# Kernel optimization log

Hardware: AMD Instinct MI355X
Metric: run time of the kernel (lower is better)

## Reference

```python
import math
import jax, jax.numpy as jnp
import numpy as np

N, E, D, H, NH, DH, EIN, EOUT, G = 30000, 480000, 128, 128, 4, 32, 16, 16, 64
EPS = 1e-5

def _leaky(x):
    return jax.nn.leaky_relu(x, 0.01)

def _graph_norm(x, batch, w, b, a):
    # torch_geometric GraphNorm: out = w * (x - a*mean) / sqrt(var + eps) + b, stats per graph
    cnt = jnp.maximum(jax.ops.segment_sum(jnp.ones((x.shape[0],), x.dtype), batch, num_segments=G), 1.0)[:, None]
    mean = jax.ops.segment_sum(x, batch, num_segments=G) / cnt
    out = x - a * mean[batch]
    var = jax.ops.segment_sum(out * out, batch, num_segments=G) / cnt
    return w * out / jnp.sqrt(var + EPS)[batch] + b

def setup_inputs() -> dict:
    key = jax.random.key(0)
    ks = jax.random.split(key, 24)
    lin = lambda k, di, do: jax.random.normal(k, (di, do), jnp.float32) * 0.02
    z = lambda d: jnp.zeros((d,), jnp.float32)
    o = lambda d: jnp.ones((d,), jnp.float32)
    return {
        "node": jax.random.normal(ks[0], (N, D), jnp.float32),
        "edge": jax.random.normal(ks[1], (E, EIN), jnp.float32),
        "coords": jax.random.normal(ks[2], (N, 3), jnp.float32),
        "Ws": lin(ks[3], D, H), "bs": z(H),
        "Wd": lin(ks[4], D, H), "bd": z(H),
        "Wv": lin(ks[5], D, H), "bv": z(H),
        "We1": lin(ks[6], EIN + 1, H), "be1": z(H),
        "We2": lin(ks[7], H, H), "be2": z(H),
        "Wun": lin(ks[8], H, H), "bun": z(H),
        "Wue": lin(ks[9], H, EOUT), "bue": z(EOUT),
        "Wg": lin(ks[10], 3 * H, H), "bg": z(H),
        "Wf1": lin(ks[11], H, H), "bf1": z(H),
        "Wf2": lin(ks[12], H, H), "bf2": z(H),
        "gn1_w": o(H), "gn1_b": z(H), "gn1_a": o(H),
        "gn2_w": o(H), "gn2_b": z(H), "gn2_a": o(H),
        "edge_index": jax.random.randint(ks[13], (2, E), 0, N),
        "batch": jnp.sort(jax.random.randint(ks[14], (N,), 0, G)),
    }

def reference(node, edge, coords, Ws, bs, Wd, bd, Wv, bv, We1, be1, We2, be2,
              Wun, bun, Wue, bue, Wg, bg, Wf1, bf1, Wf2, bf2,
              gn1_w, gn1_b, gn1_a, gn2_w, gn2_b, gn2_a, edge_index, batch):
    i, j = edge_index[0], edge_index[1]
    src = node @ Ws + bs              # [N,H]
    dst = node @ Wd + bd
    value = node @ Wv + bv
    d = coords[i] - coords[j]
    dist = jnp.sqrt(jnp.sum(d * d, axis=-1, keepdims=True) + 1e-12) * 0.1
    e = jnp.concatenate([edge, dist], axis=-1)            # [E, EIN+1]
    e = _leaky(e @ We1 + be1) @ We2 + be2                   # edge_layer (dropout=identity in eval)
    edge_key = src[j] * e
    edge_result = (dst[i] * edge_key / math.sqrt(DH)).reshape(E, NH, DH)
    scores = jnp.sum(jnp.abs(edge_result), axis=2)         # L1 norm over dh -> [E,NH]
    smax = jax.ops.segment_max(scores, i, num_segments=N)  # scatter softmax over dst nodes
    ex = jnp.exp(scores - smax[i])
    den = jax.ops.segment_sum(ex, i, num_segments=N)
    ew = (ex / den[i])[..., None]                           # [E,NH,1]
    agg = jax.ops.segment_sum(ew * value[j].reshape(E, NH, DH), i, num_segments=N).reshape(N, H)
    node_new = agg @ Wun + bun
    edge_new = edge_result.reshape(E, H) @ Wue + bue
    g = jax.nn.sigmoid(jnp.concatenate([node_new, node, node_new - node], axis=-1) @ Wg + bg)
    n1 = _graph_norm(g * node_new + node, batch, gn1_w, gn1_b, gn1_a)
    fx = _leaky(n1 @ Wf1 + bf1) @ Wf2 + bf2                 # fix_node
    n2 = _graph_norm(g * fx + n1, batch, gn2_w, gn2_b, gn2_a)
    return (n2, edge_new, coords)
```

## Files before the change

kernel.cpp:

```cpp
#include <hip/hip_runtime.h>
#include <hip/hip_bf16.h>

#define NN_ 30000
#define NE_ 480000
#define DIM 128
#define EINF 16
#define EOUTF 16
#define NG 64
#define RSQRT_DH 0.17677669529663687f

typedef unsigned short u16;
typedef __attribute__((ext_vector_type(8))) short short8;
typedef __attribute__((ext_vector_type(8))) unsigned short ushort8v;
typedef __attribute__((ext_vector_type(4))) float floatx4;

#define W_DEG     0
#define W_CUR     30000
#define W_GSUM1   60000
#define W_GSQ1    68192
#define W_GSUM2   76384
#define W_GSQ2    84576
#define W_ZEND    92768
#define W_OFF     92768
#define W_BSUM    122772
#define W_GSTART  122900
#define W_EID     122968
#define W_JC      602968
#define W_SCORES  1082968
#define W_SRCB    3002968
#define W_DSTB    4922968
#define W_VALB    6842968
#define W_A       8762968
#define W_B       12602968
#define W_C       16442968
#define W_WGC     20282968
#define W_WE2B    20315736
#define W_WPROJ   20323928

static __device__ __forceinline__ u16 f2bf(float x) {
  __hip_bfloat16 h = __float2bfloat16(x);
  return *reinterpret_cast<u16*>(&h);
}
static __device__ __forceinline__ float bf2f(u16 v) {
  unsigned int b = ((unsigned int)v) << 16;
  return __uint_as_float(b);
}

static __device__ __forceinline__ void stage32(const float* __restrict__ X,
                                               float* xsb, int row0, int tid) {
#pragma unroll
  for (int t = 0; t < 4; ++t) {
    int idx = tid + t * 256;
    int r = idx >> 5, c4 = (idx & 31) * 4;
    int row = row0 + r;
    float4 v; v.x = v.y = v.z = v.w = 0.f;
    if (row < NN_) v = *(const float4*)&X[(size_t)row * DIM + c4];
    *(float4*)&xsb[r * DIM + c4] = v;
  }
}

static __device__ __forceinline__ void mm_k128(const float* xsb, int ld,
                                               const float* __restrict__ W,
                                               float acc[4][4], int tid) {
  int cg = tid & 31, rg = tid >> 5;
  int c0 = cg * 4, r0 = rg * 4;
  for (int k = 0; k < 128; k += 4) {
    float4 w0 = *(const float4*)&W[(size_t)(k + 0) * DIM + c0];
    float4 w1 = *(const float4*)&W[(size_t)(k + 1) * DIM + c0];
    float4 w2 = *(const float4*)&W[(size_t)(k + 2) * DIM + c0];
    float4 w3 = *(const float4*)&W[(size_t)(k + 3) * DIM + c0];
#pragma unroll
    for (int u = 0; u < 4; ++u) {
      float4 xv = *(const float4*)&xsb[(r0 + u) * ld + k];
      acc[u][0] += xv.x * w0.x + xv.y * w1.x + xv.z * w2.x + xv.w * w3.x;
      acc[u][1] += xv.x * w0.y + xv.y * w1.y + xv.z * w2.y + xv.w * w3.y;
      acc[u][2] += xv.x * w0.z + xv.y * w1.z + xv.z * w2.z + xv.w * w3.z;
      acc[u][3] += xv.x * w0.w + xv.y * w1.w + xv.z * w2.w + xv.w * w3.w;
    }
  }
}

static __device__ __forceinline__ void tile_gn_stats(const float* xsb,
    const int* bg_s, int row0, int tid,
    float* __restrict__ gsum, float* __restrict__ gsq) {
  int c = tid & 127, half = tid >> 7;
  float sm = 0.f, sq = 0.f;
  int gcur = -1;
  for (int r = 0; r < 16; ++r) {
    int rl = half * 16 + r;
    int row = row0 + rl;
    if (row >= NN_) break;
    int g = bg_s[rl];
    float v = xsb[rl * DIM + c];
    if (g != gcur) {
      if (gcur >= 0) {
        atomicAdd(&gsum[gcur * DIM + c], sm);
        atomicAdd(&gsq[gcur * DIM + c], sq);
      }
      gcur = g; sm = 0.f; sq = 0.f;
    }
    sm += v; sq += v * v;
  }
  if (gcur >= 0) {
    atomicAdd(&gsum[gcur * DIM + c], sm);
    atomicAdd(&gsq[gcur * DIM + c], sq);
  }
}

__global__ void setup_kernel(const int* __restrict__ batch, int* __restrict__ gstart,
                             const float* __restrict__ Wg, float* __restrict__ Wgc,
                             const float* __restrict__ We2, u16* __restrict__ we2b,
                             const float* __restrict__ Ws, const float* __restrict__ Wd,
                             const float* __restrict__ Wv, u16* __restrict__ wproj) {
  int b = blockIdx.x, tid = threadIdx.x;
  if (b == 0) {
    int g = tid;
    if (g <= NG) {
      int lo = 0, hi = NN_;
      while (lo < hi) { int mid = (lo + hi) >> 1; if (batch[mid] < g) lo = mid + 1; else hi = mid; }
      gstart[g] = lo;
    }
  } else if (b < 129) {
    int idx = (b - 1) * 256 + tid;
    int k = idx >> 7, c = idx & 127;
    float v;
    if (k < 128) v = Wg[(size_t)k * DIM + c] + Wg[(size_t)(256 + k) * DIM + c];
    else { int kk = k - 128; v = Wg[(size_t)(128 + kk) * DIM + c] - Wg[(size_t)(256 + kk) * DIM + c]; }
    Wgc[idx] = v;
  } else if (b < 193) {
    int idx = (b - 129) * 256 + tid;
    int j = idx & 7, lane = (idx >> 3) & 63, s = (idx >> 9) & 3, T = idx >> 11;
    int k = s * 32 + ((lane >> 4) << 3) + j;
    int n = T * 16 + (lane & 15);
    we2b[idx] = f2bf(We2[(size_t)k * DIM + n]);
  } else {
    int idx = (b - 193) * 256 + tid;
    int which = idx >> 14;
    int sub = idx & 16383;
    int j = sub & 7, lane = (sub >> 3) & 63, s = (sub >> 9) & 3, T = sub >> 11;
    int k = s * 32 + ((lane >> 4) << 3) + j;
    int n = T * 16 + (lane & 15);
    int mat = which >> 1;
    const float* Wsrc = (mat == 0) ? Ws : (mat == 1) ? Wd : Wv;
    float w = Wsrc[(size_t)k * DIM + n];
    u16 h = f2bf(w);
    u16 o = (which & 1) ? f2bf(w - bf2f(h)) : h;
    wproj[which * 16384 + sub] = o;
  }
}

__global__ void deg_kernel(const int* __restrict__ EI, int* __restrict__ deg) {
  int e = blockIdx.x * 256 + threadIdx.x;
  if (e < NE_) atomicAdd(&deg[EI[e]], 1);
}

__global__ void __launch_bounds__(256) proj_kernel(
    const float* __restrict__ node, const u16* __restrict__ wproj,
    const float* __restrict__ bs, const float* __restrict__ bd,
    const float* __restrict__ bv,
    u16* __restrict__ srcb, u16* __restrict__ dstb, u16* __restrict__ valb) {
  __shared__ __align__(16) u16 ah[32 * 136];
  __shared__ __align__(16) u16 al[32 * 136];
  __shared__ __align__(16) float park[32 * 132];
  int tid = threadIdx.x, row0 = blockIdx.x * 32;
  int r2 = tid >> 3, c16 = (tid & 7) * 16;

  {
    int row = row0 + r2;
    float v[16];
    if (row < NN_) {
#pragma unroll
      for (int q = 0; q < 4; ++q) {
        float4 x = *(const float4*)&node[(size_t)row * DIM + c16 + q * 4];
        v[q * 4 + 0] = x.x; v[q * 4 + 1] = x.y;
        v[q * 4 + 2] = x.z; v[q * 4 + 3] = x.w;
      }
    } else {
#pragma unroll
      for (int q = 0; q < 16; ++q) v[q] = 0.f;
    }
#pragma unroll
    for (int h2 = 0; h2 < 2; ++h2) {
      ushort8v hh, ll;
#pragma unroll
      for (int q = 0; q < 8; ++q) {
        float x = v[h2 * 8 + q];
        u16 h = f2bf(x);
        hh[q] = h;
        ll[q] = f2bf(x - bf2f(h));
      }
      *(ushort8v*)&ah[r2 * 136 + c16 + h2 * 8] = hh;
      *(ushort8v*)&al[r2 * 136 + c16 + h2 * 8] = ll;
    }
  }
  __syncthreads();

  int wv_ = tid >> 6, lane = tid & 63;
  int mtile = wv_ & 1, nhalf = wv_ >> 1;
  int quad = lane >> 4, lrow = lane & 15;
  int m0 = mtile * 16;

  short8 afh[4], afl[4];
#pragma unroll
  for (int s = 0; s < 4; ++s) {
    afh[s] = *(const short8*)&ah[(m0 + lrow) * 136 + s * 32 + quad * 8];
    afl[s] = *(const short8*)&al[(m0 + lrow) * 136 + s * 32 + quad * 8];
  }

  const float* Bt[3] = {bs, bd, bv};
  u16* Yt[3] = {srcb, dstb, valb};
#pragma unroll 1
  for (int g3 = 0; g3 < 3; ++g3) {
    const u16* wh = wproj + (size_t)(g3 * 2 + 0) * 16384;
    const u16* wl = wproj + (size_t)(g3 * 2 + 1) * 16384;
    floatx4 dacc[4];
#pragma unroll
    for (int t = 0; t < 4; ++t) dacc[t] = (floatx4){0.f, 0.f, 0.f, 0.f};
#pragma unroll
    for (int s = 0; s < 4; ++s) {
#pragma unroll
      for (int t = 0; t < 4; ++t) {
        int T = nhalf * 4 + t;
        size_t off = (size_t)((T * 4 + s) * 64 + lane) * 8;
        short8 bh = *(const short8*)&wh[off];
        short8 bl = *(const short8*)&wl[off];
        dacc[t] = __builtin_amdgcn_mfma_f32_16x16x32_bf16(afh[s], bh, dacc[t], 0, 0, 0);
        dacc[t] = __builtin_amdgcn_mfma_f32_16x16x32_bf16(afl[s], bh, dacc[t], 0, 0, 0);
        dacc[t] = __builtin_amdgcn_mfma_f32_16x16x32_bf16(afh[s], bl, dacc[t], 0, 0, 0);
      }
    }
#pragma unroll
    for (int t = 0; t < 4; ++t) {
      int col = nhalf * 64 + t * 16 + lrow;
#pragma unroll
      for (int r = 0; r < 4; ++r)
        park[(m0 + quad * 4 + r) * 132 + col] = dacc[t][r];
    }
    __syncthreads();
    {
      int row = row0 + r2;
      if (row < NN_) {
#pragma unroll
        for (int h2 = 0; h2 < 2; ++h2) {
          ushort8v o;
#pragma unroll
          for (int q = 0; q < 8; ++q) {
            float pv = park[r2 * 132 + c16 + h2 * 8 + q] + Bt[g3][c16 + h2 * 8 + q];
            o[q] = f2bf(pv);
          }
          *(ushort8v*)&Yt[g3][(size_t)row * DIM + c16 + h2 * 8] = o;
        }
      }
    }
    __syncthreads();
  }
}

__global__ void __launch_bounds__(256) nnew_gate_kernel(
    const float* __restrict__ AGG, const float* __restrict__ NODE,
    const int* __restrict__ batch,
    const float* __restrict__ Wun, const float* __restrict__ bun,
    const float* __restrict__ Wgc, const float* __restrict__ bg,
    float* __restrict__ gsum1, float* __restrict__ gsq1,
    float* __restrict__ G, float* __restrict__ X1) {
  __shared__ __align__(16) float xs0[32 * DIM];
  __shared__ __align__(16) float xs1[32 * DIM];
  __shared__ int bg_s[32];
  int tid = threadIdx.x, row0 = blockIdx.x * 32;
  stage32(AGG, xs0, row0, tid);
  stage32(NODE, xs1, row0, tid);
  if (tid < 32) {
    int row = row0 + tid;
    bg_s[tid] = (row < NN_) ? batch[row] : 0;
  }
  __syncthreads();
  int cg = tid & 31, rg = tid >> 5, c0 = cg * 4, r0 = rg * 4;
  {
    float acc[4][4] = {};
    mm_k128(xs0, DIM, Wun, acc, tid);
    __syncthreads();
    float4 bv = *(const float4*)&bun[c0];
#pragma unroll
    for (int u = 0; u < 4; ++u) {
      float4 ov; ov.x = acc[u][0] + bv.x; ov.y = acc[u][1] + bv.y;
      ov.z = acc[u][2] + bv.z; ov.w = acc[u][3] + bv.w;
      *(float4*)&xs0[(r0 + u) * DIM + c0] = ov;
    }
  }
  __syncthreads();
  float acc[4][4] = {};
  mm_k128(xs0, DIM, Wgc, acc, tid);
  mm_k128(xs1, DIM, Wgc + 128 * DIM, acc, tid);
  float4 bv = *(const float4*)&bg[c0];
  float4 xvv[4];
#pragma unroll
  for (int u = 0; u < 4; ++u) {
    int row = row0 + r0 + u;
    float z0 = acc[u][0] + bv.x, z1 = acc[u][1] + bv.y;
    float z2 = acc[u][2] + bv.z, z3 = acc[u][3] + bv.w;
    float g0 = 1.f / (1.f + __expf(-z0));
    float g1 = 1.f / (1.f + __expf(-z1));
    float g2 = 1.f / (1.f + __expf(-z2));
    float g3 = 1.f / (1.f + __expf(-z3));
    float4 nn4 = *(const float4*)&xs0[(r0 + u) * DIM + c0];
    float4 nd4 = *(const float4*)&xs1[(r0 + u) * DIM + c0];
    float4 gv; gv.x = g0; gv.y = g1; gv.z = g2; gv.w = g3;
    float4 xv; xv.x = g0 * nn4.x + nd4.x; xv.y = g1 * nn4.y + nd4.y;
    xv.z = g2 * nn4.z + nd4.z; xv.w = g3 * nn4.w + nd4.w;
    xvv[u] = xv;
    if (row < NN_) {
      *(float4*)&G[(size_t)row * DIM + c0] = gv;
      *(float4*)&X1[(size_t)row * DIM + c0] = xv;
    }
  }
  __syncthreads();
#pragma unroll
  for (int u = 0; u < 4; ++u)
    *(float4*)&xs1[(r0 + u) * DIM + c0] = xvv[u];
  __syncthreads();
  tile_gn_stats(xs1, bg_s, row0, tid, gsum1, gsq1);
}

__global__ void __launch_bounds__(256) fx_kernel(
    const float* __restrict__ X1, const int* __restrict__ batch,
    const int* __restrict__ gstart,
    const float* __restrict__ gsum1, const float* __restrict__ gsq1,
    const float* __restrict__ g1w, const float* __restrict__ g1b,
    const float* __restrict__ g1a,
    const float* __restrict__ Wf1, const float* __restrict__ bf1,
    const float* __restrict__ Wf2, const float* __restrict__ bf2,
    const float* __restrict__ G,
    float* __restrict__ gsum2, float* __restrict__ gsq2,
    float* __restrict__ X2) {
  __shared__ __align__(16) float xs0[32 * DIM];
  __shared__ __align__(16) float xs1[32 * DIM];
  __shared__ int bg_s[32];
  int tid = threadIdx.x, row0 = blockIdx.x * 32;
  stage32(X1, xs0, row0, tid);
  if (tid < 32) {
    int row = row0 + tid;
    bg_s[tid] = (row < NN_) ? batch[row] : 0;
  }
  __syncthreads();
  int cg = tid & 31, rg = tid >> 5, c0 = cg * 4, r0 = rg * 4;
#pragma unroll
  for (int u = 0; u < 4; ++u) {
    int rl = r0 + u, row = row0 + rl;
    if (row >= NN_) continue;
    int g = bg_s[rl];
    float cnt = fmaxf((float)(gstart[g + 1] - gstart[g]), 1.f);
    float inv = 1.f / cnt;
    float4 xv = *(const float4*)&xs0[rl * DIM + c0];
    float4 sm = *(const float4*)&gsum1[g * DIM + c0];
    float4 sq = *(const float4*)&gsq1[g * DIM + c0];
    float4 av = *(const float4*)&g1a[c0];
    float4 wv = *(const float4*)&g1w[c0];
    float4 bvv = *(const float4*)&g1b[c0];
    float4 ov;
    {
      float mean = sm.x * inv, msq = sq.x * inv, am = av.x * mean;
      float var = msq - 2.f * am * mean + am * am;
      ov.x = wv.x * (xv.x - am) * rsqrtf(var + 1e-5f) + bvv.x;
    }
    {
      float mean = sm.y * inv, msq = sq.y * inv, am = av.y * mean;
      float var = msq - 2.f * am * mean + am * am;
      ov.y = wv.y * (xv.y - am) * rsqrtf(var + 1e-5f) + bvv.y;
    }
    {
      float mean = sm.z * inv, msq = sq.z * inv, am = av.z * mean;
      float var = msq - 2.f * am * mean + am * am;
      ov.z = wv.z * (xv.z - am) * rsqrtf(var + 1e-5f) + bvv.z;
    }
    {
      float mean = sm.w * inv, msq = sq.w * inv, am = av.w * mean;
      float var = msq - 2.f * am * mean + am * am;
      ov.w = wv.w * (xv.w - am) * rsqrtf(var + 1e-5f) + bvv.w;
    }
    *(float4*)&xs0[rl * DIM + c0] = ov;
  }
  __syncthreads();
  {
    float acc[4][4] = {};
    mm_k128(xs0, DIM, Wf1, acc, tid);
    float4 bv = *(const float4*)&bf1[c0];
#pragma unroll
    for (int u = 0; u < 4; ++u) {
      float t0 = acc[u][0] + bv.x, t1 = acc[u][1] + bv.y;
      float t2 = acc[u][2] + bv.z, t3 = acc[u][3] + bv.w;
      t0 = t0 > 0.f ? t0 : 0.01f * t0; t1 = t1 > 0.f ? t1 : 0.01f * t1;
      t2 = t2 > 0.f ? t2 : 0.01f * t2; t3 = t3 > 0.f ? t3 : 0.01f * t3;
      float4 ov; ov.x = t0; ov.y = t1; ov.z = t2; ov.w = t3;
      *(float4*)&xs1[(r0 + u) * DIM + c0] = ov;
    }
  }
  __syncthreads();
  float acc[4][4] = {};
  mm_k128(xs1, DIM, Wf2, acc, tid);
  float4 bv = *(const float4*)&bf2[c0];
  float4 x2v[4];
#pragma unroll
  for (int u = 0; u < 4; ++u) {
    int row = row0 + r0 + u;
    float4 nv = *(const float4*)&xs0[(r0 + u) * DIM + c0];
    float4 gv; gv.x = gv.y = gv.z = gv.w = 0.f;
    if (row < NN_) gv = *(const float4*)&G[(size_t)row * DIM + c0];
    float4 ov;
    ov.x = gv.x * (acc[u][0] + bv.x) + nv.x;
    ov.y = gv.y * (acc[u][1] + bv.y) + nv.y;
    ov.z = gv.z * (acc[u][2] + bv.z) + nv.z;
    ov.w = gv.w * (acc[u][3] + bv.w) + nv.w;
    x2v[u] = ov;
    if (row < NN_) *(float4*)&X2[(size_t)row * DIM + c0] = ov;
  }
  __syncthreads();
#pragma unroll
  for (int u = 0; u < 4; ++u)
    *(float4*)&xs1[(r0 + u) * DIM + c0] = x2v[u];
  __syncthreads();
  tile_gn_stats(xs1, bg_s, row0, tid, gsum2, gsq2);
}

__global__ void scanA_kernel(const int* __restrict__ deg, int* __restrict__ off,
                             int* __restrict__ bsum) {
  __shared__ int buf[256];
  int tid = threadIdx.x;
  int i = blockIdx.x * 256 + tid;
  int v = (i < NN_) ? deg[i] : 0;
  buf[tid] = v;
  __syncthreads();
  for (int s = 1; s < 256; s <<= 1) {
    int t = (tid >= s) ? buf[tid - s] : 0;
    __syncthreads();
    buf[tid] += t;
    __syncthreads();
  }
  if (i < NN_) off[i] = buf[tid] - v;
  if (tid == 255) bsum[blockIdx.x] = buf[255];
}

__global__ void scanB_kernel(int* __restrict__ bsum) {
  const int NBLK = (NN_ + 255) / 256;
  __shared__ int buf[128];
  int tid = threadIdx.x;
  int v = (tid < NBLK) ? bsum[tid] : 0;
  buf[tid] = v;
  __syncthreads();
  for (int s = 1; s < 128; s <<= 1) {
    int t = (tid >= s) ? buf[tid - s] : 0;
    __syncthreads();
    buf[tid] += t;
    __syncthreads();
  }
  if (tid < NBLK) bsum[tid] = buf[tid] - v;
}

__global__ void scanC_kernel(int* __restrict__ off, const int* __restrict__ bsum) {
  int i = blockIdx.x * 256 + threadIdx.x;
  if (i < NN_) off[i] += bsum[i >> 8];
  if (i == 0) off[NN_] = NE_;
}

__global__ void fill_kernel(const int* __restrict__ EI, const int* __restrict__ off,
                            int* __restrict__ cur, int* __restrict__ eidb,
                            int* __restrict__ jcsr) {
  int e = blockIdx.x * 256 + threadIdx.x;
  if (e >= NE_) return;
  int i = EI[e];
  int p = atomicAdd(&cur[i], 1);
  int pos = off[i] + p;
  eidb[pos] = e;
  jcsr[pos] = EI[NE_ + e];
}

__global__ void __launch_bounds__(256, 5) edge_kernel(
    const float* __restrict__ edgef, const float* __restrict__ coords,
    const int* __restrict__ EI, const int* __restrict__ eidb,
    const float* __restrict__ We1, const float* __restrict__ be1,
    const float* __restrict__ be2, const u16* __restrict__ we2b,
    const float* __restrict__ Wue, const float* __restrict__ bue,
    const u16* __restrict__ srcb, const u16* __restrict__ dstb,
    float* __restrict__ scores, float* __restrict__ outE) {
  __shared__ __align__(16) float regA[2816];
  __shared__ __align__(16) float ers[32 * 132];
  __shared__ float bue_s[EOUTF];
  __shared__ int ii[32], jj[32], ee[32];

  float* xs   = regA;
  u16*   hbf  = (u16*)(regA + 640);
  float* wue_s= regA;

  int tid = threadIdx.x;
  int bid = blockIdx.x;
  int bswz = (bid & 7) * (NE_ / 32 / 8) + (bid >> 3);
  int p0 = bswz * 32;

  if (tid < 32) {
    int p = p0 + tid;
    int e = eidb[p];
    ee[tid] = e;
    int i = EI[e], j = EI[NE_ + e];
    ii[tid] = i; jj[tid] = j;
    float dx = coords[i * 3 + 0] - coords[j * 3 + 0];
    float dy = coords[i * 3 + 1] - coords[j * 3 + 1];
    float dz = coords[i * 3 + 2] - coords[j * 3 + 2];
    float dist = sqrtf(dx * dx + dy * dy + dz * dz + 1e-12f) * 0.1f;
    xs[tid * 20 + 16] = dist;
  }
  if (tid < EOUTF) bue_s[tid] = bue[tid];
  __syncthreads();

  if (tid < 128) {
    int r = tid >> 2, c4 = (tid & 3) * 4;
    *(float4*)&xs[r * 20 + c4] = *(const float4*)&edgef[(size_t)ee[r] * EINF + c4];
  }
  __syncthreads();

  int cg = tid & 31, rg = tid >> 5, c0 = cg * 4, r0 = rg * 4;

  {
    float acc[4][4] = {};
    for (int k = 0; k < 16; k += 4) {
      float4 w0 = *(const float4*)&We1[(size_t)(k + 0) * DIM + c0];
      float4 w1 = *(const float4*)&We1[(size_t)(k + 1) * DIM + c0];
      float4 w2 = *(const float4*)&We1[(size_t)(k + 2) * DIM + c0];
      float4 w3 = *(const float4*)&We1[(size_t)(k + 3) * DIM + c0];
#pragma unroll
      for (int u = 0; u < 4; ++u) {
        float4 xv = *(const float4*)&xs[(r0 + u) * 20 + k];
        acc[u][0] += xv.x * w0.x + xv.y * w1.x + xv.z * w2.x + xv.w * w3.x;
        acc[u][1] += xv.x * w0.y + xv.y * w1.y + xv.z * w2.y + xv.w * w3.y;
        acc[u][2] += xv.x * w0.z + xv.y * w1.z + xv.z * w2.z + xv.w * w3.z;
        acc[u][3] += xv.x * w0.w + xv.y * w1.w + xv.z * w2.w + xv.w * w3.w;
      }
    }
    {
      float4 w4 = *(const float4*)&We1[(size_t)16 * DIM + c0];
#pragma unroll
      for (int u = 0; u < 4; ++u) {
        float xd = xs[(r0 + u) * 20 + 16];
        acc[u][0] += xd * w4.x; acc[u][1] += xd * w4.y;
        acc[u][2] += xd * w4.z; acc[u][3] += xd * w4.w;
      }
    }
    float4 b1 = *(const float4*)&be1[c0];
#pragma unroll
    for (int u = 0; u < 4; ++u) {
      float h0 = acc[u][0] + b1.x, h1 = acc[u][1] + b1.y;
      float h2 = acc[u][2] + b1.z, h3 = acc[u][3] + b1.w;
      h0 = h0 > 0.f ? h0 : 0.01f * h0; h1 = h1 > 0.f ? h1 : 0.01f * h1;
      h2 = h2 > 0.f ? h2 : 0.01f * h2; h3 = h3 > 0.f ? h3 : 0.01f * h3;
      ushort4 pk; pk.x = f2bf(h0); pk.y = f2bf(h1); pk.z = f2bf(h2); pk.w = f2bf(h3);
      *(ushort4*)&hbf[(r0 + u) * 136 + c0] = pk;
    }
  }
  __syncthreads();

  int wv = tid >> 6, lane = tid & 63;
  int mtile = wv & 1, nhalf = wv >> 1;
  int quad = lane >> 4, lrow = lane & 15;
  int m0 = mtile * 16;

  short8 afrag[4];
#pragma unroll
  for (int s = 0; s < 4; ++s)
    afrag[s] = *(const short8*)&hbf[(m0 + lrow) * 136 + s * 32 + quad * 8];
  __syncthreads();

  for (int idx = tid; idx < 16 * DIM; idx += 256) {
    int oc = idx >> 7, k = idx & 127;
    wue_s[oc * 132 + k] = Wue[(size_t)k * EOUTF + oc];
  }

// ... 140 lines not shown
  int blk = blockIdx.x;
  if (blk >= (NN_ * 32) / 256) {
    int i = (blk - (NN_ * 32) / 256) * 256 + threadIdx.x;
    if (i < NN_ * 3) OC[i] = C[i];
    return;
  }
  int idx = blk * 256 + threadIdx.x;
  int n = idx >> 5, c4 = (idx & 31) * 4;
  int g = batch[n];
  float cnt = fmaxf((float)(gstart[g + 1] - gstart[g]), 1.f);
  float inv = 1.f / cnt;
  float4 xv = *(const float4*)&X[(size_t)n * DIM + c4];
  float4 sm = *(const float4*)&gsum[g * DIM + c4];
  float4 sq = *(const float4*)&gsq[g * DIM + c4];
  float4 av = *(const float4*)&a[c4];
  float4 wv = *(const float4*)&w[c4];
  float4 bv = *(const float4*)&b[c4];
  float4 ov;
  {
    float mean = sm.x * inv, msq = sq.x * inv, am = av.x * mean;
    float var = msq - 2.f * am * mean + am * am;
    ov.x = wv.x * (xv.x - am) * rsqrtf(var + 1e-5f) + bv.x;
  }
  {
    float mean = sm.y * inv, msq = sq.y * inv, am = av.y * mean;
    float var = msq - 2.f * am * mean + am * am;
    ov.y = wv.y * (xv.y - am) * rsqrtf(var + 1e-5f) + bv.y;
  }
  {
    float mean = sm.z * inv, msq = sq.z * inv, am = av.z * mean;
    float var = msq - 2.f * am * mean + am * am;
    ov.z = wv.z * (xv.z - am) * rsqrtf(var + 1e-5f) + bv.z;
  }
  {
    float mean = sm.w * inv, msq = sq.w * inv, am = av.w * mean;
    float var = msq - 2.f * am * mean + am * am;
    ov.w = wv.w * (xv.w - am) * rsqrtf(var + 1e-5f) + bv.w;
  }
  *(float4*)&Y[(size_t)n * DIM + c4] = ov;
}

extern "C" void kernel_launch(void* const* d_in, const int* in_sizes, int n_in,
                              void* d_out, int out_size, void* d_ws, size_t ws_size,
                              hipStream_t stream) {
  (void)in_sizes; (void)n_in; (void)out_size; (void)ws_size;
  const float* node  = (const float*)d_in[0];
  const float* edgef = (const float*)d_in[1];
  const float* coords= (const float*)d_in[2];
  const float* Ws  = (const float*)d_in[3];  const float* bs  = (const float*)d_in[4];
  const float* Wd  = (const float*)d_in[5];  const float* bd  = (const float*)d_in[6];
  const float* Wv  = (const float*)d_in[7];  const float* bv  = (const float*)d_in[8];
  const float* We1 = (const float*)d_in[9];  const float* be1 = (const float*)d_in[10];
  const float* We2 = (const float*)d_in[11]; const float* be2 = (const float*)d_in[12];
  const float* Wun = (const float*)d_in[13]; const float* bun = (const float*)d_in[14];
  const float* Wue = (const float*)d_in[15]; const float* bue = (const float*)d_in[16];
  const float* Wg  = (const float*)d_in[17]; const float* bg  = (const float*)d_in[18];
  const float* Wf1 = (const float*)d_in[19]; const float* bf1 = (const float*)d_in[20];
  const float* Wf2 = (const float*)d_in[21]; const float* bf2 = (const float*)d_in[22];
  const float* g1w = (const float*)d_in[23]; const float* g1b = (const float*)d_in[24];
  const float* g1a = (const float*)d_in[25];
  const float* g2w = (const float*)d_in[26]; const float* g2b = (const float*)d_in[27];
  const float* g2a = (const float*)d_in[28];
  const int* EI    = (const int*)d_in[29];
  const int* batch = (const int*)d_in[30];
  float* out = (float*)d_out;

  int*   wsi = (int*)d_ws;
  float* wsf = (float*)d_ws;
  int* deg    = wsi + W_DEG;
  int* cur    = wsi + W_CUR;
  int* offs   = wsi + W_OFF;
  int* bsum   = wsi + W_BSUM;
  int* gstart = wsi + W_GSTART;
  int* eidb   = wsi + W_EID;
  int* jcsr   = wsi + W_JC;
  float* gsum1 = wsf + W_GSUM1; float* gsq1 = wsf + W_GSQ1;
  float* gsum2 = wsf + W_GSUM2; float* gsq2 = wsf + W_GSQ2;
  float* scores_ = wsf + W_SCORES;
  u16* srcb = (u16*)(wsf + W_SRCB);
  u16* dstb = (u16*)(wsf + W_DSTB);
  u16* valb = (u16*)(wsf + W_VALB);
  float* A = wsf + W_A;
  float* B = wsf + W_B;
  float* wgc_ = wsf + W_WGC;
  u16*   we2b = (u16*)(wsf + W_WE2B);
  u16*   wproj = (u16*)(wsf + W_WPROJ);

  float* outE = out + (size_t)NN_ * DIM;
  float* outC = out + (size_t)NN_ * DIM + (size_t)NE_ * EOUTF;

  hipMemsetAsync(d_ws, 0, (size_t)W_ZEND * sizeof(int), stream);
  setup_kernel<<<577, 256, 0, stream>>>(batch, gstart, Wg, wgc_, We2, we2b,
                                        Ws, Wd, Wv, wproj);
  deg_kernel<<<(NE_ + 255) / 256, 256, 0, stream>>>(EI, deg);
  scanA_kernel<<<(NN_ + 255) / 256, 256, 0, stream>>>(deg, offs, bsum);
  scanB_kernel<<<1, 128, 0, stream>>>(bsum);
  scanC_kernel<<<(NN_ + 255) / 256, 256, 0, stream>>>(offs, bsum);
  fill_kernel<<<(NE_ + 255) / 256, 256, 0, stream>>>(EI, offs, cur, eidb, jcsr);
  proj_kernel<<<(NN_ + 31) / 32, 256, 0, stream>>>(node, wproj, bs, bd, bv,
                                                   srcb, dstb, valb);
  edge_kernel<<<NE_ / 32, 256, 0, stream>>>(edgef, coords, EI, eidb, We1, be1,
                                            be2, we2b, Wue, bue,
                                            srcb, dstb, scores_, outE);
  agg_kernel<<<NN_ / 4, 256, 0, stream>>>(valb, scores_, offs, jcsr, A);
  nnew_gate_kernel<<<(NN_ + 31) / 32, 256, 0, stream>>>(A, node, batch, Wun, bun,
                                                        wgc_, bg, gsum1, gsq1, B, A);
  fx_kernel<<<(NN_ + 31) / 32, 256, 0, stream>>>(A, batch, gstart, gsum1, gsq1,
                                                 g1w, g1b, g1a, Wf1, bf1, Wf2, bf2,
                                                 B, gsum2, gsq2, A);
  gn_apply_kernel<<<(NN_ * 32) / 256 + (NN_ * 3 + 255) / 256, 256, 0, stream>>>(
      A, batch, gstart, gsum2, gsq2, g2w, g2b, g2a, out, coords, outC);
}
```

Baseline: 574.0 us.

## Move node-side GEMMs to split-bf16 MFMA and tighten edge kernel LDS

Replaces the scalar fp32 mm_k128 GEMMs in the gate and fix_node kernels with bf16 MFMA using a hi/lo split of activations and weights, keeping close to fp32 accuracy with three MFMAs per product. Setup now pre-swizzles Wun, the combined gate weights and Wf1/Wf2 into MFMA fragment layout. The edge kernel's shared buffers are merged into one smaller allocation and its occupancy hint raised from 5 to 6 blocks. The split-bf16 scheme adds extra MFMA work and conversion cost, and the larger setup grid adds a little fixed overhead.

```diff
diff --git a/kernel.cpp b/kernel.cpp
--- a/kernel.cpp
+++ b/kernel.cpp
@@ -46,41 +46,7 @@
   return __uint_as_float(b);
 }
 
-static __device__ __forceinline__ void stage32(const float* __restrict__ X,
-                                               float* xsb, int row0, int tid) {
-#pragma unroll
-  for (int t = 0; t < 4; ++t) {
-    int idx = tid + t * 256;
-    int r = idx >> 5, c4 = (idx & 31) * 4;
-    int row = row0 + r;
-    float4 v; v.x = v.y = v.z = v.w = 0.f;
-    if (row < NN_) v = *(const float4*)&X[(size_t)row * DIM + c4];
-    *(float4*)&xsb[r * DIM + c4] = v;
-  }
-}
-
-static __device__ __forceinline__ void mm_k128(const float* xsb, int ld,
-                                               const float* __restrict__ W,
-                                               float acc[4][4], int tid) {
-  int cg = tid & 31, rg = tid >> 5;
-  int c0 = cg * 4, r0 = rg * 4;
-  for (int k = 0; k < 128; k += 4) {
-    float4 w0 = *(const float4*)&W[(size_t)(k + 0) * DIM + c0];
-    float4 w1 = *(const float4*)&W[(size_t)(k + 1) * DIM + c0];
-    float4 w2 = *(const float4*)&W[(size_t)(k + 2) * DIM + c0];
-    float4 w3 = *(const float4*)&W[(size_t)(k + 3) * DIM + c0];
-#pragma unroll
-    for (int u = 0; u < 4; ++u) {
-      float4 xv = *(const float4*)&xsb[(r0 + u) * ld + k];
-      acc[u][0] += xv.x * w0.x + xv.y * w1.x + xv.z * w2.x + xv.w * w3.x;
-      acc[u][1] += xv.x * w0.y + xv.y * w1.y + xv.z * w2.y + xv.w * w3.y;
-      acc[u][2] += xv.x * w0.z + xv.y * w1.z + xv.z * w2.z + xv.w * w3.z;
-      acc[u][3] += xv.x * w0.w + xv.y * w1.w + xv.z * w2.w + xv.w * w3.w;
-    }
-  }
-}
-
-static __device__ __forceinline__ void tile_gn_stats(const float* xsb,
+static __device__ __forceinline__ void tile_gn_stats(const float* xsb, int ld,
     const int* bg_s, int row0, int tid,
     float* __restrict__ gsum, float* __restrict__ gsq) {
   int c = tid & 127, half = tid >> 7;
@@ -91,7 +57,7 @@
     int row = row0 + rl;
     if (row >= NN_) break;
     int g = bg_s[rl];
-    float v = xsb[rl * DIM + c];
+    float v = xsb[rl * ld + c];
     if (g != gcur) {
       if (gcur >= 0) {
         atomicAdd(&gsum[gcur * DIM + c], sm);
@@ -108,10 +74,12 @@
 }
 
 __global__ void setup_kernel(const int* __restrict__ batch, int* __restrict__ gstart,
-                             const float* __restrict__ Wg, float* __restrict__ Wgc,
+                             const float* __restrict__ Wg,
                              const float* __restrict__ We2, u16* __restrict__ we2b,
                              const float* __restrict__ Ws, const float* __restrict__ Wd,
-                             const float* __restrict__ Wv, u16* __restrict__ wproj) {
+                             const float* __restrict__ Wv, const float* __restrict__ Wun,
+                             const float* __restrict__ Wf1, const float* __restrict__ Wf2,
+                             u16* __restrict__ wfrag) {
   int b = blockIdx.x, tid = threadIdx.x;
   if (b == 0) {
     int g = tid;
@@ -120,32 +88,30 @@
       while (lo < hi) { int mid = (lo + hi) >> 1; if (batch[mid] < g) lo = mid + 1; else hi = mid; }
       gstart[g] = lo;
     }
-  } else if (b < 129) {
+  } else if (b < 65) {
     int idx = (b - 1) * 256 + tid;
-    int k = idx >> 7, c = idx & 127;
-    float v;
-    if (k < 128) v = Wg[(size_t)k * DIM + c] + Wg[(size_t)(256 + k) * DIM + c];
-    else { int kk = k - 128; v = Wg[(size_t)(128 + kk) * DIM + c] - Wg[(size_t)(256 + kk) * DIM + c]; }
-    Wgc[idx] = v;
-  } else if (b < 193) {
-    int idx = (b - 129) * 256 + tid;
     int j = idx & 7, lane = (idx >> 3) & 63, s = (idx >> 9) & 3, T = idx >> 11;
     int k = s * 32 + ((lane >> 4) << 3) + j;
     int n = T * 16 + (lane & 15);
     we2b[idx] = f2bf(We2[(size_t)k * DIM + n]);
   } else {
-    int idx = (b - 193) * 256 + tid;
+    int idx = (b - 65) * 256 + tid;
     int which = idx >> 14;
     int sub = idx & 16383;
     int j = sub & 7, lane = (sub >> 3) & 63, s = (sub >> 9) & 3, T = sub >> 11;
     int k = s * 32 + ((lane >> 4) << 3) + j;
     int n = T * 16 + (lane & 15);
     int mat = which >> 1;
-    const float* Wsrc = (mat == 0) ? Ws : (mat == 1) ? Wd : Wv;
-    float w = Wsrc[(size_t)k * DIM + n];
+    float w;
+    if (mat == 4) w = Wg[(size_t)k * DIM + n] + Wg[(size_t)(256 + k) * DIM + n];
+    else if (mat == 5) w = Wg[(size_t)(128 + k) * DIM + n] - Wg[(size_t)(256 + k) * DIM + n];
+    else {
+      const float* Wsrc = (mat == 0) ? Ws : (mat == 1) ? Wd : (mat == 2) ? Wv
+                        : (mat == 3) ? Wun : (mat == 6) ? Wf1 : Wf2;
+      w = Wsrc[(size_t)k * DIM + n];
+    }
     u16 h = f2bf(w);
-    u16 o = (which & 1) ? f2bf(w - bf2f(h)) : h;
-    wproj[which * 16384 + sub] = o;
+    wfrag[(size_t)which * 16384 + sub] = (which & 1) ? f2bf(w - bf2f(h)) : h;
   }
 }
 
@@ -155,7 +121,7 @@
 }
 
 __global__ void __launch_bounds__(256) proj_kernel(
-    const float* __restrict__ node, const u16* __restrict__ wproj,
+    const float* __restrict__ node, const u16* __restrict__ wfrag,
     const float* __restrict__ bs, const float* __restrict__ bd,
     const float* __restrict__ bv,
     u16* __restrict__ srcb, u16* __restrict__ dstb, u16* __restrict__ valb) {
@@ -211,8 +177,8 @@
   u16* Yt[3] = {srcb, dstb, valb};
 #pragma unroll 1
   for (int g3 = 0; g3 < 3; ++g3) {
-    const u16* wh = wproj + (size_t)(g3 * 2 + 0) * 16384;
-    const u16* wl = wproj + (size_t)(g3 * 2 + 1) * 16384;
+    const u16* wh = wfrag + (size_t)(g3 * 2 + 0) * 16384;
+    const u16* wl = wfrag + (size_t)(g3 * 2 + 1) * 16384;
     floatx4 dacc[4];
 #pragma unroll
     for (int t = 0; t < 4; ++t) dacc[t] = (floatx4){0.f, 0.f, 0.f, 0.f};
@@ -258,67 +224,166 @@
 
 __global__ void __launch_bounds__(256) nnew_gate_kernel(
     const float* __restrict__ AGG, const float* __restrict__ NODE,
-    const int* __restrict__ batch,
-    const float* __restrict__ Wun, const float* __restrict__ bun,
-    const float* __restrict__ Wgc, const float* __restrict__ bg,
+    const int* __restrict__ batch, const u16* __restrict__ wfrag,
+    const float* __restrict__ bun, const float* __restrict__ bg,
     float* __restrict__ gsum1, float* __restrict__ gsq1,
     float* __restrict__ G, float* __restrict__ X1) {
-  __shared__ __align__(16) float xs0[32 * DIM];
-  __shared__ __align__(16) float xs1[32 * DIM];
+  __shared__ __align__(16) u16 a_h[32 * 136];
+  __shared__ __align__(16) u16 a_l[32 * 136];
+  __shared__ __align__(16) u16 n_h[32 * 136];
+  __shared__ __align__(16) u16 n_l[32 * 136];
+  __shared__ __align__(16) float park[32 * 132];
   __shared__ int bg_s[32];
   int tid = threadIdx.x, row0 = blockIdx.x * 32;
-  stage32(AGG, xs0, row0, tid);
-  stage32(NODE, xs1, row0, tid);
-  if (tid < 32) {
-    int row = row0 + tid;
-    bg_s[tid] = (row < NN_) ? batch[row] : 0;
-  }
-  __syncthreads();
-  int cg = tid & 31, rg = tid >> 5, c0 = cg * 4, r0 = rg * 4;
-  {
-    float acc[4][4] = {};
-    mm_k128(xs0, DIM, Wun, acc, tid);
-    __syncthreads();
-    float4 bv = *(const float4*)&bun[c0];
-#pragma unroll
-    for (int u = 0; u < 4; ++u) {
-      float4 ov; ov.x = acc[u][0] + bv.x; ov.y = acc[u][1] + bv.y;
-      ov.z = acc[u][2] + bv.z; ov.w = acc[u][3] + bv.w;
-      *(float4*)&xs0[(r0 + u) * DIM + c0] = ov;
-    }
-  }
-  __syncthreads();
-  float acc[4][4] = {};
-  mm_k128(xs0, DIM, Wgc, acc, tid);
-  mm_k128(xs1, DIM, Wgc + 128 * DIM, acc, tid);
-  float4 bv = *(const float4*)&bg[c0];
-  float4 xvv[4];
-#pragma unroll
-  for (int u = 0; u < 4; ++u) {
-    int row = row0 + r0 + u;
-    float z0 = acc[u][0] + bv.x, z1 = acc[u][1] + bv.y;
-    float z2 = acc[u][2] + bv.z, z3 = acc[u][3] + bv.w;
-    float g0 = 1.f / (1.f + __expf(-z0));
-    float g1 = 1.f / (1.f + __expf(-z1));
-    float g2 = 1.f / (1.f + __expf(-z2));
-    float g3 = 1.f / (1.f + __expf(-z3));
-    float4 nn4 = *(const float4*)&xs0[(r0 + u) * DIM + c0];
-    float4 nd4 = *(const float4*)&xs1[(r0 + u) * DIM + c0];
-    float4 gv; gv.x = g0; gv.y = g1; gv.z = g2; gv.w = g3;
-    float4 xv; xv.x = g0 * nn4.x + nd4.x; xv.y = g1 * nn4.y + nd4.y;
-    xv.z = g2 * nn4.z + nd4.z; xv.w = g3 * nn4.w + nd4.w;
-    xvv[u] = xv;
+  int r2 = tid >> 3, c16 = (tid & 7) * 16;
+  if (tid < 32) bg_s[tid] = (row0 + tid < NN_) ? batch[row0 + tid] : 0;
+
+  {
+    int row = row0 + r2;
+    float va[16], vn[16];
     if (row < NN_) {
-      *(float4*)&G[(size_t)row * DIM + c0] = gv;
-      *(float4*)&X1[(size_t)row * DIM + c0] = xv;
-    }
-  }
-  __syncthreads();
-#pragma unroll
-  for (int u = 0; u < 4; ++u)
-    *(float4*)&xs1[(r0 + u) * DIM + c0] = xvv[u];
-  __syncthreads();
-  tile_gn_stats(xs1, bg_s, row0, tid, gsum1, gsq1);
+#pragma unroll
+      for (int q = 0; q < 4; ++q) {
+        float4 xa = *(const float4*)&AGG[(size_t)row * DIM + c16 + q * 4];
+        float4 xn = *(const float4*)&NODE[(size_t)row * DIM + c16 + q * 4];
+        va[q * 4 + 0] = xa.x; va[q * 4 + 1] = xa.y; va[q * 4 + 2] = xa.z; va[q * 4 + 3] = xa.w;
+        vn[q * 4 + 0] = xn.x; vn[q * 4 + 1] = xn.y; vn[q * 4 + 2] = xn.z; vn[q * 4 + 3] = xn.w;
+      }
+    } else {
+#pragma unroll
+      for (int q = 0; q < 16; ++q) { va[q] = 0.f; vn[q] = 0.f; }
+    }
+#pragma unroll
+    for (int h2 = 0; h2 < 2; ++h2) {
+      ushort8v ah8, al8, nh8, nl8;
+#pragma unroll
+      for (int q = 0; q < 8; ++q) {
+        float x = va[h2 * 8 + q];
+        u16 h = f2bf(x); ah8[q] = h; al8[q] = f2bf(x - bf2f(h));
+        float y = vn[h2 * 8 + q];
+        u16 hy = f2bf(y); nh8[q] = hy; nl8[q] = f2bf(y - bf2f(hy));
+      }
+      *(ushort8v*)&a_h[r2 * 136 + c16 + h2 * 8] = ah8;
+      *(ushort8v*)&a_l[r2 * 136 + c16 + h2 * 8] = al8;
+      *(ushort8v*)&n_h[r2 * 136 + c16 + h2 * 8] = nh8;
+      *(ushort8v*)&n_l[r2 * 136 + c16 + h2 * 8] = nl8;
+    }
+  }
+  __syncthreads();
+
+  int wv_ = tid >> 6, lane = tid & 63;
+  int mtile = wv_ & 1, nhalf = wv_ >> 1;
+  int quad = lane >> 4, lrow = lane & 15;
+  int m0 = mtile * 16;
+
+  const u16* WunH = wfrag + (size_t)6 * 16384;
+  const u16* WunL = wfrag + (size_t)7 * 16384;
+  const u16* G0H  = wfrag + (size_t)8 * 16384;
+  const u16* G0L  = wfrag + (size_t)9 * 16384;
+  const u16* G1H  = wfrag + (size_t)10 * 16384;
+  const u16* G1L  = wfrag + (size_t)11 * 16384;
+
+  {
+    short8 fh[4], fl[4];
+#pragma unroll
+    for (int s = 0; s < 4; ++s) {
+      fh[s] = *(const short8*)&a_h[(m0 + lrow) * 136 + s * 32 + quad * 8];
+      fl[s] = *(const short8*)&a_l[(m0 + lrow) * 136 + s * 32 + quad * 8];
+    }
+    floatx4 d1[4];
+#pragma unroll
+    for (int t = 0; t < 4; ++t) d1[t] = (floatx4){0.f, 0.f, 0.f, 0.f};
+#pragma unroll
+    for (int s = 0; s < 4; ++s) {
+#pragma unroll
+      for (int t = 0; t < 4; ++t) {
+        int T = nhalf * 4 + t;
+        size_t off = (size_t)((T * 4 + s) * 64 + lane) * 8;
+        short8 bh = *(const short8*)&WunH[off];
+        short8 bl = *(const short8*)&WunL[off];
+        d1[t] = __builtin_amdgcn_mfma_f32_16x16x32_bf16(fh[s], bh, d1[t], 0, 0, 0);
+        d1[t] = __builtin_amdgcn_mfma_f32_16x16x32_bf16(fl[s], bh, d1[t], 0, 0, 0);
+        d1[t] = __builtin_amdgcn_mfma_f32_16x16x32_bf16(fh[s], bl, d1[t], 0, 0, 0);
+      }
+    }
+#pragma unroll
+    for (int t = 0; t < 4; ++t) {
+      int col = nhalf * 64 + t * 16 + lrow;
+#pragma unroll
+      for (int r = 0; r < 4; ++r)
+        park[(m0 + quad * 4 + r) * 132 + col] = d1[t][r];
+    }
+  }
+  __syncthreads();
+
+  {
+#pragma unroll
+    for (int h2 = 0; h2 < 2; ++h2) {
+      ushort8v hh, ll;
+#pragma unroll
+      for (int q = 0; q < 8; ++q) {
+        float x = park[r2 * 132 + c16 + h2 * 8 + q] + bun[c16 + h2 * 8 + q];
+        u16 h = f2bf(x); hh[q] = h; ll[q] = f2bf(x - bf2f(h));
+      }
+      *(ushort8v*)&a_h[r2 * 136 + c16 + h2 * 8] = hh;
+      *(ushort8v*)&a_l[r2 * 136 + c16 + h2 * 8] = ll;
+    }
+  }
+  __syncthreads();
+
+  {
+    short8 mh[4], ml[4], ph[4], pl[4];
+#pragma unroll
+    for (int s = 0; s < 4; ++s) {
+      mh[s] = *(const short8*)&a_h[(m0 + lrow) * 136 + s * 32 + quad * 8];
+      ml[s] = *(const short8*)&a_l[(m0 + lrow) * 136 + s * 32 + quad * 8];
+      ph[s] = *(const short8*)&n_h[(m0 + lrow) * 136 + s * 32 + quad * 8];
+      pl[s] = *(const short8*)&n_l[(m0 + lrow) * 136 + s * 32 + quad * 8];
+    }
+    floatx4 d2[4];
+#pragma unroll
+    for (int t = 0; t < 4; ++t) d2[t] = (floatx4){0.f, 0.f, 0.f, 0.f};
+#pragma unroll
+    for (int s = 0; s < 4; ++s) {
+#pragma unroll
+      for (int t = 0; t < 4; ++t) {
+        int T = nhalf * 4 + t;
+        size_t off = (size_t)((T * 4 + s) * 64 + lane) * 8;
+        short8 g0h = *(const short8*)&G0H[off];
+        short8 g0l = *(const short8*)&G0L[off];
+        short8 g1h = *(const short8*)&G1H[off];
+        short8 g1l = *(const short8*)&G1L[off];
+        d2[t] = __builtin_amdgcn_mfma_f32_16x16x32_bf16(mh[s], g0h, d2[t], 0, 0, 0);
+        d2[t] = __builtin_amdgcn_mfma_f32_16x16x32_bf16(ml[s], g0h, d2[t], 0, 0, 0);
+        d2[t] = __builtin_amdgcn_mfma_f32_16x16x32_bf16(mh[s], g0l, d2[t], 0, 0, 0);
+        d2[t] = __builtin_amdgcn_mfma_f32_16x16x32_bf16(ph[s], g1h, d2[t], 0, 0, 0);
+        d2[t] = __builtin_amdgcn_mfma_f32_16x16x32_bf16(pl[s], g1h, d2[t], 0, 0, 0);
+        d2[t] = __builtin_amdgcn_mfma_f32_16x16x32_bf16(ph[s], g1l, d2[t], 0, 0, 0);
+      }
+    }
+#pragma unroll
+    for (int t = 0; t < 4; ++t) {
+      int col = nhalf * 64 + t * 16 + lrow;
+      float bgv = bg[col], bunv = bun[col];
+#pragma unroll
+      for (int r = 0; r < 4; ++r) {
+        int erow = m0 + quad * 4 + r;
+        int row = row0 + erow;
+        float z = d2[t][r] + bgv;
+        float gg = 1.f / (1.f + __expf(-z));
+        float nn = park[erow * 132 + col] + bunv;
+        float nodev = bf2f(n_h[erow * 136 + col]) + bf2f(n_l[erow * 136 + col]);
+        float x1 = gg * nn + nodev;
+        park[erow * 132 + col] = x1;
+        if (row < NN_) {
+          G[(size_t)row * DIM + col] = gg;
+          X1[(size_t)row * DIM + col] = x1;
+        }
+      }
+    }
+  }
+  __syncthreads();
+  tile_gn_stats(park, 132, bg_s, row0, tid, gsum1, gsq1);
 }
 
 __global__ void __launch_bounds__(256) fx_kernel(
@@ -326,99 +391,156 @@
     const int* __restrict__ gstart,
     const float* __restrict__ gsum1, const float* __restrict__ gsq1,
     const float* __restrict__ g1w, const float* __restrict__ g1b,
-    const float* __restrict__ g1a,
-    const float* __restrict__ Wf1, const float* __restrict__ bf1,
-    const float* __restrict__ Wf2, const float* __restrict__ bf2,
+    const float* __restrict__ g1a, const u16* __restrict__ wfrag,
+    const float* __restrict__ bf1, const float* __restrict__ bf2,
     const float* __restrict__ G,
     float* __restrict__ gsum2, float* __restrict__ gsq2,
     float* __restrict__ X2) {
-  __shared__ __align__(16) float xs0[32 * DIM];
-  __shared__ __align__(16) float xs1[32 * DIM];
+  __shared__ __align__(16) u16 a_h[32 * 136];
+  __shared__ __align__(16) u16 a_l[32 * 136];
+  __shared__ __align__(16) float n1s[32 * 132];
   __shared__ int bg_s[32];
   int tid = threadIdx.x, row0 = blockIdx.x * 32;
-  stage32(X1, xs0, row0, tid);
-  if (tid < 32) {
-    int row = row0 + tid;
-    bg_s[tid] = (row < NN_) ? batch[row] : 0;
-  }
-  __syncthreads();
-  int cg = tid & 31, rg = tid >> 5, c0 = cg * 4, r0 = rg * 4;
-#pragma unroll
-  for (int u = 0; u < 4; ++u) {
-    int rl = r0 + u, row = row0 + rl;
-    if (row >= NN_) continue;
-    int g = bg_s[rl];
-    float cnt = fmaxf((float)(gstart[g + 1] - gstart[g]), 1.f);
+  int r2 = tid >> 3, c16 = (tid & 7) * 16;
+  if (tid < 32) bg_s[tid] = (row0 + tid < NN_) ? batch[row0 + tid] : 0;
+
+  {
+    int row = row0 + r2;
+    int gi = (row < NN_) ? batch[row] : 0;
+    float cnt = fmaxf((float)(gstart[gi + 1] - gstart[gi]), 1.f);
     float inv = 1.f / cnt;
-    float4 xv = *(const float4*)&xs0[rl * DIM + c0];
-    float4 sm = *(const float4*)&gsum1[g * DIM + c0];
-    float4 sq = *(const float4*)&gsq1[g * DIM + c0];
-    float4 av = *(const float4*)&g1a[c0];
-    float4 wv = *(const float4*)&g1w[c0];
-    float4 bvv = *(const float4*)&g1b[c0];
-    float4 ov;
-    {
-      float mean = sm.x * inv, msq = sq.x * inv, am = av.x * mean;
+    float v[16];
+    if (row < NN_) {
+#pragma unroll
+      for (int q = 0; q < 4; ++q) {
+        float4 x = *(const float4*)&X1[(size_t)row * DIM + c16 + q * 4];
+        v[q * 4 + 0] = x.x; v[q * 4 + 1] = x.y;
+        v[q * 4 + 2] = x.z; v[q * 4 + 3] = x.w;
+      }
+    } else {
+#pragma unroll
+      for (int q = 0; q < 16; ++q) v[q] = 0.f;
+    }
+#pragma unroll
+    for (int q0 = 0; q0 < 16; ++q0) {
+      int c = c16 + q0;
+      float sm = gsum1[gi * DIM + c], sq = gsq1[gi * DIM + c];
+      float mean = sm * inv, msq = sq * inv, am = g1a[c] * mean;
       float var = msq - 2.f * am * mean + am * am;
-      ov.x = wv.x * (xv.x - am) * rsqrtf(var + 1e-5f) + bvv.x;
-    }
-    {
-      float mean = sm.y * inv, msq = sq.y * inv, am = av.y * mean;
-      float var = msq - 2.f * am * mean + am * am;
-      ov.y = wv.y * (xv.y - am) * rsqrtf(var + 1e-5f) + bvv.y;
-    }
-    {
-      float mean = sm.z * inv, msq = sq.z * inv, am = av.z * mean;
-      float var = msq - 2.f * am * mean + am * am;
-      ov.z = wv.z * (xv.z - am) * rsqrtf(var + 1e-5f) + bvv.z;
-    }
-    {
-      float mean = sm.w * inv, msq = sq.w * inv, am = av.w * mean;
-      float var = msq - 2.f * am * mean + am * am;
-      ov.w = wv.w * (xv.w - am) * rsqrtf(var + 1e-5f) + bvv.w;
-    }
-    *(float4*)&xs0[rl * DIM + c0] = ov;
-  }
-  __syncthreads();
-  {
-    float acc[4][4] = {};
-    mm_k128(xs0, DIM, Wf1, acc, tid);
-    float4 bv = *(const float4*)&bf1[c0];
-#pragma unroll
-    for (int u = 0; u < 4; ++u) {
-      float t0 = acc[u][0] + bv.x, t1 = acc[u][1] + bv.y;
-      float t2 = acc[u][2] + bv.z, t3 = acc[u][3] + bv.w;
-      t0 = t0 > 0.f ? t0 : 0.01f * t0; t1 = t1 > 0.f ? t1 : 0.01f * t1;
-      t2 = t2 > 0.f ? t2 : 0.01f * t2; t3 = t3 > 0.f ? t3 : 0.01f * t3;
-      float4 ov; ov.x = t0; ov.y = t1; ov.z = t2; ov.w = t3;
-      *(float4*)&xs1[(r0 + u) * DIM + c0] = ov;
-    }
-  }
-  __syncthreads();
-  float acc[4][4] = {};
-  mm_k128(xs1, DIM, Wf2, acc, tid);
-  float4 bv = *(const float4*)&bf2[c0];
-  float4 x2v[4];
-#pragma unroll
-  for (int u = 0; u < 4; ++u) {
-    int row = row0 + r0 + u;
-    float4 nv = *(const float4*)&xs0[(r0 + u) * DIM + c0];
-    float4 gv; gv.x = gv.y = gv.z = gv.w = 0.f;
-    if (row < NN_) gv = *(const float4*)&G[(size_t)row * DIM + c0];
-    float4 ov;
-    ov.x = gv.x * (acc[u][0] + bv.x) + nv.x;
-    ov.y = gv.y * (acc[u][1] + bv.y) + nv.y;
-    ov.z = gv.z * (acc[u][2] + bv.z) + nv.z;
-    ov.w = gv.w * (acc[u][3] + bv.w) + nv.w;
-    x2v[u] = ov;
-    if (row < NN_) *(float4*)&X2[(size_t)row * DIM + c0] = ov;
-  }
-  __syncthreads();
-#pragma unroll
-  for (int u = 0; u < 4; ++u)
-    *(float4*)&xs1[(r0 + u) * DIM + c0] = x2v[u];
-  __syncthreads();
-  tile_gn_stats(xs1, bg_s, row0, tid, gsum2, gsq2);
+      v[q0] = g1w[c] * (v[q0] - am) * rsqrtf(var + 1e-5f) + g1b[c];
+    }
+#pragma unroll
+    for (int q = 0; q < 4; ++q) {
+      float4 o; o.x = v[q * 4 + 0]; o.y = v[q * 4 + 1];
+      o.z = v[q * 4 + 2]; o.w = v[q * 4 + 3];
+      *(float4*)&n1s[r2 * 132 + c16 + q * 4] = o;
+    }
+#pragma unroll
+    for (int h2 = 0; h2 < 2; ++h2) {
+      ushort8v hh, ll;
+#pragma unroll
+      for (int q = 0; q < 8; ++q) {
+        float x = v[h2 * 8 + q];
+        u16 h = f2bf(x); hh[q] = h; ll[q] = f2bf(x - bf2f(h));
+      }
+      *(ushort8v*)&a_h[r2 * 136 + c16 + h2 * 8] = hh;
+      *(ushort8v*)&a_l[r2 * 136 + c16 + h2 * 8] = ll;
+    }
+  }
+  __syncthreads();
+
+  int wv_ = tid >> 6, lane = tid & 63;
+  int mtile = wv_ & 1, nhalf = wv_ >> 1;
+  int quad = lane >> 4, lrow = lane & 15;
+  int m0 = mtile * 16;
+
+  const u16* F1H = wfrag + (size_t)12 * 16384;
+  const u16* F1L = wfrag + (size_t)13 * 16384;
+  const u16* F2H = wfrag + (size_t)14 * 16384;
+  const u16* F2L = wfrag + (size_t)15 * 16384;
+
+  short8 fh[4], fl[4];
+#pragma unroll
+  for (int s = 0; s < 4; ++s) {
+    fh[s] = *(const short8*)&a_h[(m0 + lrow) * 136 + s * 32 + quad * 8];
+    fl[s] = *(const short8*)&a_l[(m0 + lrow) * 136 + s * 32 + quad * 8];
+  }
+  __syncthreads();
+
+  {
+    floatx4 d1[4];
+#pragma unroll
+    for (int t = 0; t < 4; ++t) d1[t] = (floatx4){0.f, 0.f, 0.f, 0.f};
+#pragma unroll
+    for (int s = 0; s < 4; ++s) {
+#pragma unroll
+      for (int t = 0; t < 4; ++t) {
+        int T = nhalf * 4 + t;
+        size_t off = (size_t)((T * 4 + s) * 64 + lane) * 8;
+        short8 bh = *(const short8*)&F1H[off];
+        short8 bl = *(const short8*)&F1L[off];
+        d1[t] = __builtin_amdgcn_mfma_f32_16x16x32_bf16(fh[s], bh, d1[t], 0, 0, 0);
+        d1[t] = __builtin_amdgcn_mfma_f32_16x16x32_bf16(fl[s], bh, d1[t], 0, 0, 0);
+        d1[t] = __builtin_amdgcn_mfma_f32_16x16x32_bf16(fh[s], bl, d1[t], 0, 0, 0);
+      }
+    }
+#pragma unroll
+    for (int t = 0; t < 4; ++t) {
+      int col = nhalf * 64 + t * 16 + lrow;
+      float b1v = bf1[col];
+#pragma unroll
+      for (int r = 0; r < 4; ++r) {
+        int erow = m0 + quad * 4 + r;
+        float tt = d1[t][r] + b1v;
+        tt = tt > 0.f ? tt : 0.01f * tt;
+        u16 h = f2bf(tt);
+        a_h[erow * 136 + col] = h;
+        a_l[erow * 136 + col] = f2bf(tt - bf2f(h));
+      }
+    }
+  }
+  __syncthreads();
+
+  {
+    short8 th[4], tl[4];
+#pragma unroll
+    for (int s = 0; s < 4; ++s) {
+      th[s] = *(const short8*)&a_h[(m0 + lrow) * 136 + s * 32 + quad * 8];
+      tl[s] = *(const short8*)&a_l[(m0 + lrow) * 136 + s * 32 + quad * 8];
+    }
+    floatx4 d2[4];
+#pragma unroll
+    for (int t = 0; t < 4; ++t) d2[t] = (floatx4){0.f, 0.f, 0.f, 0.f};
+#pragma unroll
+    for (int s = 0; s < 4; ++s) {
+#pragma unroll
+      for (int t = 0; t < 4; ++t) {
+        int T = nhalf * 4 + t;
+        size_t off = (size_t)((T * 4 + s) * 64 + lane) * 8;
+        short8 bh = *(const short8*)&F2H[off];
+        short8 bl = *(const short8*)&F2L[off];
+        d2[t] = __builtin_amdgcn_mfma_f32_16x16x32_bf16(th[s], bh, d2[t], 0, 0, 0);
+        d2[t] = __builtin_amdgcn_mfma_f32_16x16x32_bf16(tl[s], bh, d2[t], 0, 0, 0);
+        d2[t] = __builtin_amdgcn_mfma_f32_16x16x32_bf16(th[s], bl, d2[t], 0, 0, 0);
+      }
+    }
+#pragma unroll
+    for (int t = 0; t < 4; ++t) {
+      int col = nhalf * 64 + t * 16 + lrow;
+      float b2v = bf2[col];
+#pragma unroll
+      for (int r = 0; r < 4; ++r) {
+        int erow = m0 + quad * 4 + r;
+        int row = row0 + erow;
+        float gg = (row < NN_) ? G[(size_t)row * DIM + col] : 0.f;
+        float x2 = gg * (d2[t][r] + b2v) + n1s[erow * 132 + col];
+        n1s[erow * 132 + col] = x2;
+        if (row < NN_) X2[(size_t)row * DIM + col] = x2;
+      }
+    }
+  }
+  __syncthreads();
+  tile_gn_stats(n1s, 132, bg_s, row0, tid, gsum2, gsq2);
 }
 
 __global__ void scanA_kernel(const int* __restrict__ deg, int* __restrict__ off,
@@ -473,7 +595,7 @@
   jcsr[pos] = EI[NE_ + e];
 }
 
-__global__ void __launch_bounds__(256, 5) edge_kernel(
+__global__ void __launch_bounds__(256, 6) edge_kernel(
     const float* __restrict__ edgef, const float* __restrict__ coords,
     const int* __restrict__ EI, const int* __restrict__ eidb,
     const float* __restrict__ We1, const float* __restrict__ be1,
@@ -481,14 +603,14 @@
     const float* __restrict__ Wue, const float* __restrict__ bue,
     const u16* __restrict__ srcb, const u16* __restrict__ dstb,
     float* __restrict__ scores, float* __restrict__ outE) {
-  __shared__ __align__(16) float regA[2816];
-  __shared__ __align__(16) float ers[32 * 132];
+  __shared__ __align__(16) float sbuf[6336];
   __shared__ float bue_s[EOUTF];
   __shared__ int ii[32], jj[32], ee[32];
 
-  float* xs   = regA;
-  u16*   hbf  = (u16*)(regA + 640);
-  float* wue_s= regA;
+  float* xs    = sbuf;
+  u16*   hbf   = (u16*)(sbuf + 640);
+  float* wue_s = sbuf;
+  float* ers   = sbuf + 2112;
 
   int tid = threadIdx.x;
   int bid = blockIdx.x;
@@ -795,31 +917,30 @@
   u16* valb = (u16*)(wsf + W_VALB);
   float* A = wsf + W_A;
   float* B = wsf + W_B;
-  float* wgc_ = wsf + W_WGC;
-  u16*   we2b = (u16*)(wsf + W_WE2B);
-  u16*   wproj = (u16*)(wsf + W_WPROJ);
+  u16*   we2b  = (u16*)(wsf + W_WE2B);
+  u16*   wfrag = (u16*)(wsf + W_WPROJ);
 
   float* outE = out + (size_t)NN_ * DIM;
   float* outC = out + (size_t)NN_ * DIM + (size_t)NE_ * EOUTF;
 
   hipMemsetAsync(d_ws, 0, (size_t)W_ZEND * sizeof(int), stream);
-  setup_kernel<<<577, 256, 0, stream>>>(batch, gstart, Wg, wgc_, We2, we2b,
-                                        Ws, Wd, Wv, wproj);
+  setup_kernel<<<1089, 256, 0, stream>>>(batch, gstart, Wg, We2, we2b,
+                                         Ws, Wd, Wv, Wun, Wf1, Wf2, wfrag);
   deg_kernel<<<(NE_ + 255) / 256, 256, 0, stream>>>(EI, deg);
   scanA_kernel<<<(NN_ + 255) / 256, 256, 0, stream>>>(deg, offs, bsum);
   scanB_kernel<<<1, 128, 0, stream>>>(bsum);
   scanC_kernel<<<(NN_ + 255) / 256, 256, 0, stream>>>(offs, bsum);
   fill_kernel<<<(NE_ + 255) / 256, 256, 0, stream>>>(EI, offs, cur, eidb, jcsr);
-  proj_kernel<<<(NN_ + 31) / 32, 256, 0, stream>>>(node, wproj, bs, bd, bv,
+  proj_kernel<<<(NN_ + 31) / 32, 256, 0, stream>>>(node, wfrag, bs, bd, bv,
                                                    srcb, dstb, valb);
   edge_kernel<<<NE_ / 32, 256, 0, stream>>>(edgef, coords, EI, eidb, We1, be1,
                                             be2, we2b, Wue, bue,
                                             srcb, dstb, scores_, outE);
   agg_kernel<<<NN_ / 4, 256, 0, stream>>>(valb, scores_, offs, jcsr, A);
-  nnew_gate_kernel<<<(NN_ + 31) / 32, 256, 0, stream>>>(A, node, batch, Wun, bun,
-                                                        wgc_, bg, gsum1, gsq1, B, A);
+  nnew_gate_kernel<<<(NN_ + 31) / 32, 256, 0, stream>>>(A, node, batch, wfrag,
+                                                        bun, bg, gsum1, gsq1, B, A);
   fx_kernel<<<(NN_ + 31) / 32, 256, 0, stream>>>(A, batch, gstart, gsum1, gsq1,
-                                                 g1w, g1b, g1a, Wf1, bf1, Wf2, bf2,
+                                                 g1w, g1b, g1a, wfrag, bf1, bf2,
                                                  B, gsum2, gsq2, A);
   gn_apply_kernel<<<(NN_ * 32) / 256 + (NN_ * 3 + 255) / 256, 256, 0, stream>>>(
       A, batch, gstart, gsum2, gsq2, g2w, g2b, g2a, out, coords, outC);
```

New measurement: 531.9 us. 7.3% less time.
